# Kernel tuning notes

Hardware: AMD Instinct MI355X
Metric: run time of the kernel (lower is better)

Reference implementation:

```python
import jax, jax.numpy as jnp
import numpy as np
import math

B, S, P, G = 8, 512, 64, 64
E, GE = 768, 32          # sub_embed_dim, gene_embed_dim
HD = E // 2              # sub_head_dim = 384
L = P * G
LAMBDA_INIT = 0.8 - 0.6 * math.exp(-0.3 * 0)  # depth=0 -> 0.2
SCALING = HD ** -0.5


def setup_inputs() -> dict:
    key0 = jax.random.key(0)
    ks = jax.random.split(key0, 12)
    init = 0.02
    return {
        "query": jax.random.normal(ks[0], (B, S, E), jnp.float32),
        "key": jax.random.normal(ks[1], (B, P, G, GE), jnp.float32),
        "query_mask": jax.random.bernoulli(ks[2], 0.9, (B, S)),
        "key_mask": jax.random.bernoulli(ks[3], 0.9, (B, P, G)),
        # weights stored [in, out] so y = x @ W (equiv to torch Linear no-bias)
        "Wq": jax.random.normal(ks[4], (E, E), jnp.float32) * init,
        "Wkv": jax.random.normal(ks[5], (GE, 2 * E), jnp.float32) * init,
        "Wout": jax.random.normal(ks[6], (E, E), jnp.float32) * init,
        "lambda_q1": jax.random.normal(ks[7], (HD,), jnp.float32) * 0.1,
        "lambda_k1": jax.random.normal(ks[8], (HD,), jnp.float32) * 0.1,
        "lambda_q2": jax.random.normal(ks[9], (HD,), jnp.float32) * 0.1,
        "lambda_k2": jax.random.normal(ks[10], (HD,), jnp.float32) * 0.1,
        "ln_weight": jnp.ones((E,), jnp.float32),  # RMSNorm affine weight (2*HD = E)
    }


def reference(query, key, query_mask, key_mask, Wq, Wkv, Wout,
              lambda_q1, lambda_k1, lambda_q2, lambda_k2, ln_weight):
    # Projections
    Q = query @ Wq                                   # [B,S,E]
    KV = key.reshape(B, L, GE) @ Wkv                 # [B,L,2E]
    K = KV[..., :E]                                  # [B,L,E]
    V = KV[..., E:]                                  # [B,L,E] (= 2*HD)

    # Split into 2 heads of dim HD
    Qh = Q.reshape(B, S, 2, HD).transpose(0, 2, 1, 3) * SCALING   # [B,2,S,HD]
    Kh = K.reshape(B, L, 2, HD).transpose(0, 2, 1, 3)             # [B,2,L,HD]

    # Combined mask [B,S,L]
    mask = query_mask[:, :, None] & key_mask.reshape(B, L)[:, None, :]

    # Dual attention scores + stable softmax (eps=1e-8 on denominator)
    scores = jnp.einsum('bhsd,bhld->bhsl', Qh, Kh)                # [B,2,S,L]
    scores = jnp.where(mask[:, None], scores, -1e20)
    m = jnp.max(scores, axis=-1, keepdims=True)
    p = jnp.exp(scores - m)
    attn = p / (jnp.sum(p, axis=-1, keepdims=True) + 1e-8)

    # Differential combination
    lam = (jnp.exp(jnp.sum(lambda_q1 * lambda_k1))
           - jnp.exp(jnp.sum(lambda_q2 * lambda_k2)) + LAMBDA_INIT)
    diff = attn[:, 0] - lam * attn[:, 1]                          # [B,S,L]
    diff = diff - jnp.min(diff, axis=-1, keepdims=True) + 1e-20
    diff = jnp.where(mask, diff, 0.0)

    # Value contraction: [B,S,L] @ [B,L,E] -> [B,S,E]
    attn_out = jnp.einsum('bsl,ble->bse', diff, V)

    # RMSNorm (eps=1e-5, affine) then scale by (1 - lambda_init)
    ms = jnp.mean(attn_out * attn_out, axis=-1, keepdims=True)
    attn_out = attn_out * jax.lax.rsqrt(ms + 1e-5) * ln_weight
    attn_out = attn_out * (1.0 - LAMBDA_INIT)

    out = attn_out @ Wout                                         # [B,S,E]
    return out, diff.reshape(B, S, P, G)
```

## Files before the change

### kernel.cpp

```cpp
#include <hip/hip_runtime.h>
#include <math.h>

#define LAM_INIT 0.2f
#define ONE_MINUS_LAM 0.8f
#define SCALING_F 0.05103103630798288f

typedef _Float16 h2 __attribute__((ext_vector_type(2)));

#if defined(__has_builtin)
#if __has_builtin(__builtin_amdgcn_fdot2)
#define FDOT2(a, b, c) __builtin_amdgcn_fdot2((a), (b), (c), false)
#endif
#endif
#ifndef FDOT2
#define FDOT2(a, b, c) ((float)(a).x * (float)(b).x + ((float)(a).y * (float)(b).y + (c)))
#endif

__device__ inline float waveMax(float v) {
#pragma unroll
    for (int o = 32; o > 0; o >>= 1) v = fmaxf(v, __shfl_xor(v, o));
    return v;
}
__device__ inline float waveMin(float v) {
#pragma unroll
    for (int o = 32; o > 0; o >>= 1) v = fminf(v, __shfl_xor(v, o));
    return v;
}
__device__ inline float waveSum(float v) {
#pragma unroll
    for (int o = 32; o > 0; o >>= 1) v += __shfl_xor(v, o);
    return v;
}

__global__ __launch_bounds__(256) void k01_prep(
    const float* __restrict__ key, const float* __restrict__ Wq,
    const float* __restrict__ Wkv, const float* __restrict__ Wout,
    const float* __restrict__ lq1, const float* __restrict__ lk1,
    const float* __restrict__ lq2, const float* __restrict__ lk2,
    const float* __restrict__ ln,
    unsigned* __restrict__ keyThU, float* __restrict__ Wcp,
    float* __restrict__ Wvp, float* __restrict__ lam)
{
    int blk = blockIdx.x;
    int tid = threadIdx.x;
    if (blk < 128) {
        int b  = blk >> 4;
        int l0 = (blk & 15) << 8;
        __shared__ float tile[256 * 33];
        const float* kp = key + ((size_t)b * 4096 + l0) * 32;
#pragma unroll
        for (int q = 0; q < 32; ++q) {
            int idx = tid + (q << 8);
            int r = idx >> 5, g = idx & 31;
            tile[r * 33 + g] = kp[idx];
        }
        __syncthreads();
#pragma unroll
        for (int gp = 0; gp < 16; ++gp) {
            h2 v;
            v.x = (_Float16)tile[tid * 33 + 2 * gp];
            v.y = (_Float16)tile[tid * 33 + 2 * gp + 1];
            keyThU[((size_t)(b * 16 + gp)) * 4096 + l0 + tid] =
                __builtin_bit_cast(unsigned, v);
        }
    } else if (blk < 512) {
        int bb = blk - 128;
        int kc = bb & 1;
        int ob = bb >> 1;
        int idx = ob * 256 + tid;
        int e  = idx >> 6;
        int hg = idx & 63;
        int h = hg >> 5, g = hg & 31;
        const float4* wqr = (const float4*)(Wq  + (size_t)e * 768 + h * 384 + kc * 192);
        const float4* wkr = (const float4*)(Wkv + (size_t)g * 1536 + h * 384 + kc * 192);
        float s0 = 0.f, s1 = 0.f;
#pragma unroll 4
        for (int d = 0; d < 48; d += 2) {
            float4 a0 = wqr[d],   b0 = wkr[d];
            float4 a1 = wqr[d+1], b1 = wkr[d+1];
            s0 += a0.x*b0.x + a0.y*b0.y + a0.z*b0.z + a0.w*b0.w;
            s1 += a1.x*b1.x + a1.y*b1.y + a1.z*b1.z + a1.w*b1.w;
        }
        Wcp[kc * 49152 + idx] = (s0 + s1) * SCALING_F;
    } else if (blk < 1280) {
        int bb = blk - 512;
        int kc = bb / 96;
        int ob = bb - kc * 96;
        int idx = ob * 256 + tid;
        int g = idx / 768;
        int e = idx - g * 768;
        const float* wvr = Wkv + (size_t)g * 1536 + 768;
        int c0 = kc * 96;
        float s0 = 0.f, s1 = 0.f;
#pragma unroll 4
        for (int c = c0; c < c0 + 96; c += 2) {
            s0 += wvr[c]   * ln[c]   * Wout[(size_t)c * 768 + e];
            s1 += wvr[c+1] * ln[c+1] * Wout[(size_t)(c+1) * 768 + e];
        }
        Wvp[kc * 24576 + idx] = s0 + s1;
    } else {
        float s1 = 0.f, s2 = 0.f;
        for (int d = tid; d < 384; d += 256) {
            s1 += lq1[d] * lk1[d];
            s2 += lq2[d] * lk2[d];
        }
        s1 = waveSum(s1);
        s2 = waveSum(s2);
        __shared__ float r1[4], r2[4];
        int wid = tid >> 6, lane = tid & 63;
        if (lane == 0) { r1[wid] = s1; r2[wid] = s2; }
        __syncthreads();
        if (tid == 0) {
            float a  = r1[0] + r1[1] + r1[2] + r1[3];
            float b2 = r2[0] + r2[1] + r2[2] + r2[3];
            lam[0] = expf(a) - expf(b2) + LAM_INIT;
        }
    }
}

__global__ __launch_bounds__(256) void k2_qt(
    const float* __restrict__ query, const float* __restrict__ Wcp,
    const float* __restrict__ Wvp, float* __restrict__ Wvo,
    float* __restrict__ Qtp)
{
    int blk = blockIdx.x;
    int tid = threadIdx.x;
    if (blk >= 512) {
        int idx = (blk - 512) * 256 + tid;
        float s = 0.f;
#pragma unroll
        for (int kc = 0; kc < 8; ++kc) s += Wvp[kc * 24576 + idx];
        Wvo[idx] = s;
        return;
    }
    int kc = blk >> 7;
    int mt = blk & 127;
    int m0 = mt * 32;
    __shared__ __align__(16) float As[64 * 33];
    __shared__ __align__(16) float Bs[64 * 64];

    int tm = tid >> 5;
    int tn = tid & 31;
    float acc[4][2];
#pragma unroll
    for (int r = 0; r < 4; ++r) { acc[r][0] = 0.f; acc[r][1] = 0.f; }

    for (int ch = 0; ch < 3; ++ch) {
        int k0 = kc * 192 + ch * 64;
        __syncthreads();
#pragma unroll
        for (int q = 0; q < 2; ++q) {
            int f = tid + q * 256;
            int m = f >> 4, kq = f & 15;
            float4 v = *(const float4*)&query[(size_t)(m0 + m) * 768 + k0 + kq * 4];
            As[(kq * 4 + 0) * 33 + m] = v.x;
            As[(kq * 4 + 1) * 33 + m] = v.y;
            As[(kq * 4 + 2) * 33 + m] = v.z;
            As[(kq * 4 + 3) * 33 + m] = v.w;
        }
#pragma unroll
        for (int q = 0; q < 4; ++q) {
            int f = tid + q * 256;
            int kk = f >> 4, n4 = f & 15;
            float4 a = *(const float4*)&Wcp[(size_t)(k0 + kk) * 64 + n4 * 4];
            float4 b = *(const float4*)&Wcp[49152 + (size_t)(k0 + kk) * 64 + n4 * 4];
            float4 s; s.x = a.x + b.x; s.y = a.y + b.y; s.z = a.z + b.z; s.w = a.w + b.w;
            *(float4*)&Bs[kk * 64 + n4 * 4] = s;
        }
        __syncthreads();
#pragma unroll 8
        for (int kk = 0; kk < 64; ++kk) {
            float4 a = *(const float4*)&As[kk * 33 + tm * 4];
            float2 b = *(const float2*)&Bs[kk * 64 + tn * 2];
            acc[0][0] += a.x * b.x; acc[0][1] += a.x * b.y;
            acc[1][0] += a.y * b.x; acc[1][1] += a.y * b.y;
            acc[2][0] += a.z * b.x; acc[2][1] += a.z * b.y;
            acc[3][0] += a.w * b.x; acc[3][1] += a.w * b.y;
        }
    }
#pragma unroll
    for (int r = 0; r < 4; ++r) {
        float2 o; o.x = acc[r][0]; o.y = acc[r][1];
        *(float2*)&Qtp[(size_t)kc * 262144 + (size_t)(m0 + tm * 4 + r) * 64 + tn * 2] = o;
    }
}

__global__ __launch_bounds__(512, 4) void k3_attn(
    const float* __restrict__ Qtp, const unsigned* __restrict__ keyThU,
    const int* __restrict__ qmask, const int* __restrict__ kmask,
    const float* __restrict__ lamp, float* __restrict__ diffO)
{
    int blk = blockIdx.x;
    int b  = blk >> 7;
    int s0 = (blk & 127) * 4;
    int tid = threadIdx.x;
    int lane = tid & 63, wid = tid >> 6;

    __shared__ __align__(16) unsigned qt_th[128];
    __shared__ float red[64];

    if (tid < 128) {
        int ts = tid >> 5;
        int h  = (tid >> 4) & 1;
        int gp = tid & 15;
        size_t row = (size_t)(b * 512 + s0 + ts) * 64;
        int col = h * 32 + 2 * gp;
        float v0 = 0.f, v1 = 0.f;
#pragma unroll
        for (int kc = 0; kc < 4; ++kc) {
            v0 += Qtp[(size_t)kc * 262144 + row + col];
            v1 += Qtp[(size_t)kc * 262144 + row + col + 1];
        }
        h2 hv; hv.x = (_Float16)v0; hv.y = (_Float16)v1;
        qt_th[gp * 8 + ts * 2 + h] = __builtin_bit_cast(unsigned, hv);
    }
    int qm[4];
#pragma unroll
    for (int ts = 0; ts < 4; ++ts) qm[ts] = qmask[b * 512 + s0 + ts];
    float lam = lamp[0];

    unsigned kmb = 0;
#pragma unroll
    for (int c = 0; c < 2; ++c) {
        int4 km = *(const int4*)(kmask + b * 4096 + c * 2048 + tid * 4);
        if (km.x) kmb |= 1u << (c * 4 + 0);
        if (km.y) kmb |= 1u << (c * 4 + 1);
        if (km.z) kmb |= 1u << (c * 4 + 2);
        if (km.w) kmb |= 1u << (c * 4 + 3);
    }
    __syncthreads();

    float p[2][4][8];
#pragma unroll
    for (int h = 0; h < 2; ++h)
#pragma unroll
        for (int ts = 0; ts < 4; ++ts)
#pragma unroll
            for (int i = 0; i < 8; ++i) p[h][ts][i] = 0.f;

    const unsigned* kt = keyThU + (size_t)b * 16 * 4096 + tid * 4;
    for (int gp = 0; gp < 16; ++gp) {
        uint4 q0 = *(const uint4*)&qt_th[gp * 8];
        uint4 q1 = *(const uint4*)&qt_th[gp * 8 + 4];
        h2 qv[8];
        qv[0] = __builtin_bit_cast(h2, q0.x); qv[1] = __builtin_bit_cast(h2, q0.y);
        qv[2] = __builtin_bit_cast(h2, q0.z); qv[3] = __builtin_bit_cast(h2, q0.w);
        qv[4] = __builtin_bit_cast(h2, q1.x); qv[5] = __builtin_bit_cast(h2, q1.y);
        qv[6] = __builtin_bit_cast(h2, q1.z); qv[7] = __builtin_bit_cast(h2, q1.w);
        const unsigned* kg = kt + (size_t)gp * 4096;
#pragma unroll
        for (int c = 0; c < 2; ++c) {
            uint4 kv = *(const uint4*)(kg + c * 2048);
            h2 k0 = __builtin_bit_cast(h2, kv.x);
            h2 k1 = __builtin_bit_cast(h2, kv.y);
            h2 k2 = __builtin_bit_cast(h2, kv.z);
            h2 k3 = __builtin_bit_cast(h2, kv.w);
#pragma unroll
            for (int ts = 0; ts < 4; ++ts)
#pragma unroll
                for (int h = 0; h < 2; ++h) {
                    h2 q = qv[ts * 2 + h];
                    p[h][ts][c*4+0] = FDOT2(k0, q, p[h][ts][c*4+0]);
                    p[h][ts][c*4+1] = FDOT2(k1, q, p[h][ts][c*4+1]);
                    p[h][ts][c*4+2] = FDOT2(k2, q, p[h][ts][c*4+2]);
                    p[h][ts][c*4+3] = FDOT2(k3, q, p[h][ts][c*4+3]);
                }
        }
    }

#pragma unroll
    for (int h = 0; h < 2; ++h)
#pragma unroll
        for (int ts = 0; ts < 4; ++ts)
#pragma unroll
            for (int i = 0; i < 8; ++i) {
                bool ok = qm[ts] && ((kmb >> i) & 1u);
                p[h][ts][i] = ok ? p[h][ts][i] : -1e20f;
            }

    float mrow[2][4];
#pragma unroll
    for (int h = 0; h < 2; ++h)
#pragma unroll
        for (int ts = 0; ts < 4; ++ts) {
            float v = -3.4e38f;
#pragma unroll
            for (int i = 0; i < 8; ++i) v = fmaxf(v, p[h][ts][i]);
            v = waveMax(v);
            if (lane == 0) red[(h * 4 + ts) * 8 + wid] = v;
        }
    __syncthreads();
#pragma unroll
    for (int h = 0; h < 2; ++h)
#pragma unroll
        for (int ts = 0; ts < 4; ++ts) {
            int r = (h * 4 + ts) * 8;
            float v = red[r];
#pragma unroll
            for (int w = 1; w < 8; ++w) v = fmaxf(v, red[r + w]);
            mrow[h][ts] = v;
        }
    __syncthreads();

    float inv[2][4];
#pragma unroll
    for (int h = 0; h < 2; ++h)
#pragma unroll
        for (int ts = 0; ts < 4; ++ts) {
            float s = 0.f;
#pragma unroll
            for (int i = 0; i < 8; ++i) {
                float e2 = __expf(p[h][ts][i] - mrow[h][ts]);
                p[h][ts][i] = e2;
                s += e2;
            }
            s = waveSum(s);
            if (lane == 0) red[(h * 4 + ts) * 8 + wid] = s;
        }
    __syncthreads();
#pragma unroll
    for (int h = 0; h < 2; ++h)
#pragma unroll
        for (int ts = 0; ts < 4; ++ts) {
            int r = (h * 4 + ts) * 8;
            float s = red[r];
#pragma unroll
            for (int w = 1; w < 8; ++w) s += red[r + w];
            inv[h][ts] = 1.0f / (s + 1e-8f);
        }
    __syncthreads();

    float mn[4];
#pragma unroll
    for (int ts = 0; ts < 4; ++ts) {
        float v = 3.4e38f;
#pragma unroll
        for (int i = 0; i < 8; ++i) {
            float d = p[0][ts][i] * inv[0][ts] - lam * (p[1][ts][i] * inv[1][ts]);
            p[0][ts][i] = d;
            v = fminf(v, d);
        }
        v = waveMin(v);
        if (lane == 0) red[ts * 8 + wid] = v;
    }
    __syncthreads();
#pragma unroll
    for (int ts = 0; ts < 4; ++ts) {
        int r = ts * 8;
        float v = red[r];
#pragma unroll
        for (int w = 1; w < 8; ++w) v = fminf(v, red[r + w]);
        mn[ts] = v;
    }

#pragma unroll
    for (int ts = 0; ts < 4; ++ts) {
        size_t base = (size_t)(b * 512 + s0 + ts) * 4096 + tid * 4;
#pragma unroll
        for (int c = 0; c < 2; ++c) {
            float4 o;
            float v0 = p[0][ts][c*4+0] - mn[ts] + 1e-20f;
            float v1 = p[0][ts][c*4+1] - mn[ts] + 1e-20f;
            float v2 = p[0][ts][c*4+2] - mn[ts] + 1e-20f;
            float v3 = p[0][ts][c*4+3] - mn[ts] + 1e-20f;
            o.x = (qm[ts] && ((kmb >> (c*4+0)) & 1u)) ? v0 : 0.f;
            o.y = (qm[ts] && ((kmb >> (c*4+1)) & 1u)) ? v1 : 0.f;
            o.z = (qm[ts] && ((kmb >> (c*4+2)) & 1u)) ? v2 : 0.f;
            o.w = (qm[ts] && ((kmb >> (c*4+3)) & 1u)) ? v3 : 0.f;
            *(float4*)(diffO + base + c * 2048) = o;
        }
    }
}

__global__ __launch_bounds__(256) void k4_T(
    const float* __restrict__ diff, const float* __restrict__ key,
    float* __restrict__ P)
{
    int blk = blockIdx.x;
    int rt = blk & 63, kc = blk >> 6;
    int row0 = rt << 6;
    int b = row0 >> 9;
    int l0 = kc << 9;
    int tid = threadIdx.x;
    int tx = tid & 7;
    int ty = tid >> 3;
    int g0 = tx * 4;

    __shared__ __align__(16) float Ks[256][32];

    float acc[2][4];
#pragma unroll
    for (int r = 0; r < 2; ++r)
#pragma unroll
        for (int c2 = 0; c2 < 4; ++c2) acc[r][c2] = 0.f;

    for (int ph = 0; ph < 2; ++ph) {
        int lp = l0 + ph * 256;
        __syncthreads();
#pragma unroll
        for (int q = 0; q < 32; ++q) {
            int idx = tid + (q << 8);
            int r = idx >> 5, g = idx & 31;
            Ks[r][g] = key[((size_t)(b * 4096 + lp + r)) * 32 + g];
        }
        __syncthreads();

        for (int j4 = 0; j4 < 64; ++j4) {
            int l = lp + j4 * 4;
            float4 dv[2];
#pragma unroll
            for (int r = 0; r < 2; ++r)
                dv[r] = *(const float4*)(diff + (size_t)(row0 + ty * 2 + r) * 4096 + l);
#pragma unroll
            for (int jj = 0; jj < 4; ++jj) {
                float4 kq = *(const float4*)&Ks[j4 * 4 + jj][g0];
#pragma unroll
                for (int r = 0; r < 2; ++r) {
                    float d = (jj == 0) ? dv[r].x : (jj == 1) ? dv[r].y : (jj == 2) ? dv[r].z : dv[r].w;
                    acc[r][0] += d * kq.x;
                    acc[r][1] += d * kq.y;
                    acc[r][2] += d * kq.z;
                    acc[r][3] += d * kq.w;
                }
            }
        }
    }
#pragma unroll
    for (int r = 0; r < 2; ++r) {
        float4 o; o.x = acc[r][0]; o.y = acc[r][1]; o.z = acc[r][2]; o.w = acc[r][3];
        *(float4*)&P[(size_t)kc * 131072 + (size_t)(row0 + ty * 2 + r) * 32 + g0] = o;
    }
}

__global__ __launch_bounds__(256) void k5_out(
    const float* __restrict__ P, const float* __restrict__ Wkv,
    const float* __restrict__ Wvo, float* __restrict__ out)
{
    int row0 = blockIdx.x * 8;
    int tid = threadIdx.x;
    int wid = tid >> 6, lane = tid & 63;
    __shared__ __align__(16) float Ts[8][32];
    __shared__ float red[8][4];
    __shared__ float rs_s[8];

    {
        int r = tid >> 5, g = tid & 31;
        float s = 0.f;
#pragma unroll
        for (int kc = 0; kc < 8; ++kc)
            s += P[(size_t)kc * 131072 + (size_t)(row0 + r) * 32 + g];
        Ts[r][g] = s;
    }
    __syncthreads();

    float ssq[8];
#pragma unroll
    for (int r = 0; r < 8; ++r) ssq[r] = 0.f;

#pragma unroll
    for (int ec = 0; ec < 3; ++ec) {
        int e = tid + ec * 256;
        float wv[32];
#pragma unroll
        for (int g = 0; g < 32; ++g) wv[g] = Wkv[(size_t)g * 1536 + 768 + e];
#pragma unroll
        for (int r = 0; r < 8; ++r) {
            float a = 0.f;
#pragma unroll
            for (int g = 0; g < 32; ++g) a += Ts[r][g] * wv[g];
            ssq[r] += a * a;
        }
    }
#pragma unroll
    for (int r = 0; r < 8; ++r) {
        float v = waveSum(ssq[r]);
        if (lane == 0) red[r][wid] = v;
    }
    __syncthreads();
    if (tid < 8) {
        float s = red[tid][0] + red[tid][1] + red[tid][2] + red[tid][3];
        float ms = s * (1.0f / 768.0f);
        rs_s[tid] = rsqrtf(ms + 1e-5f) * ONE_MINUS_LAM;
    }
    __syncthreads();

#pragma unroll
    for (int ec = 0; ec < 3; ++ec) {
        int e = tid + ec * 256;
        float wo[32];
#pragma unroll
        for (int g = 0; g < 32; ++g) wo[g] = Wvo[(size_t)g * 768 + e];
#pragma unroll
        for (int r = 0; r < 8; ++r) {
            float o = 0.f;
#pragma unroll
            for (int g = 0; g < 32; ++g) o += Ts[r][g] * wo[g];
            out[(size_t)(row0 + r) * 768 + e] = o * rs_s[r];
        }
    }
}

extern "C" void kernel_launch(void* const* d_in, const int* in_sizes, int n_in,
                              void* d_out, int out_size, void* d_ws, size_t ws_size,
                              hipStream_t stream) {
    (void)in_sizes; (void)n_in; (void)out_size; (void)ws_size;
    const float* query = (const float*)d_in[0];
    const float* key   = (const float*)d_in[1];
    const int*   qmask = (const int*)d_in[2];
    const int*   kmask = (const int*)d_in[3];
    const float* Wq    = (const float*)d_in[4];
    const float* Wkv   = (const float*)d_in[5];
    const float* Wout  = (const float*)d_in[6];
    const float* lq1   = (const float*)d_in[7];
    const float* lk1   = (const float*)d_in[8];
    const float* lq2   = (const float*)d_in[9];
    const float* lk2   = (const float*)d_in[10];
    const float* ln    = (const float*)d_in[11];

    float* out  = (float*)d_out;
    float* diff = out + 3145728;

    float* ws      = (float*)d_ws;
    float* Wcp     = ws;
    float* Wvo     = ws + 98304;
    float* Wvp     = ws + 122880;
    float* lam     = ws + 319488;
    unsigned* keyThU = (unsigned*)(ws + 319552);
    float* Qtp     = ws + 843840;
    float* P       = Qtp;

    k01_prep<<<1281, 256, 0, stream>>>(key, Wq, Wkv, Wout, lq1, lk1, lq2, lk2, ln,
                                       keyThU, Wcp, Wvp, lam);
    k2_qt<<<608, 256, 0, stream>>>(query, Wcp, Wvp, Wvo, Qtp);
    k3_attn<<<1024, 512, 0, stream>>>(Qtp, keyThU, qmask, kmask, lam, diff);
    k4_T<<<512, 256, 0, stream>>>(diff, key, P);
    k5_out<<<512, 256, 0, stream>>>(P, Wkv, Wvo, out);
}
```

Measured before the change: 234.7 us.

## Drop softmax max reduction, halve query rows per attention block, prefetch keys

The attention kernel now handles 2 query rows per block instead of 4 and launches twice as many blocks. It removes the row-max reduction and its block barriers by exponentiating raw scores directly, zeroing masked entries instead of using a -1e20 fill. It also register-prefetches the next key group and uses nontemporal loads and stores for the Q partials and the diff output. Skipping the max subtraction assumes scores stay small enough not to overflow exp. Fewer rows per block means each block re-reads the full key tile, which doubles key traffic.

Measured after the change: 439.0 us. 1.87x slower.

```diff
diff --git a/kernel.cpp b/kernel.cpp
--- a/kernel.cpp
+++ b/kernel.cpp
@@ -6,6 +6,7 @@
 #define SCALING_F 0.05103103630798288f
 
 typedef _Float16 h2 __attribute__((ext_vector_type(2)));
+typedef float f4 __attribute__((ext_vector_type(4)));
 
 #if defined(__has_builtin)
 #if __has_builtin(__builtin_amdgcn_fdot2)
@@ -16,11 +17,6 @@
 #define FDOT2(a, b, c) ((float)(a).x * (float)(b).x + ((float)(a).y * (float)(b).y + (c)))
 #endif
 
-__device__ inline float waveMax(float v) {
-#pragma unroll
-    for (int o = 32; o > 0; o >>= 1) v = fmaxf(v, __shfl_xor(v, o));
-    return v;
-}
 __device__ inline float waveMin(float v) {
 #pragma unroll
     for (int o = 32; o > 0; o >>= 1) v = fminf(v, __shfl_xor(v, o));
@@ -191,15 +187,16 @@
     const float* __restrict__ lamp, float* __restrict__ diffO)
 {
     int blk = blockIdx.x;
-    int b  = blk >> 7;
-    int s0 = (blk & 127) * 4;
+    int b  = blk >> 8;
+    int s0 = (blk & 255) * 2;
     int tid = threadIdx.x;
     int lane = tid & 63, wid = tid >> 6;
 
-    __shared__ __align__(16) unsigned qt_th[128];
-    __shared__ float red[64];
-
-    if (tid < 128) {
+    __shared__ __align__(16) unsigned qt_th[64];
+    __shared__ float redS[32];
+    __shared__ float redM[16];
+
+    if (tid < 64) {
         int ts = tid >> 5;
         int h  = (tid >> 4) & 1;
         int gp = tid & 15;
@@ -208,15 +205,15 @@
         float v0 = 0.f, v1 = 0.f;
 #pragma unroll
         for (int kc = 0; kc < 4; ++kc) {
-            v0 += Qtp[(size_t)kc * 262144 + row + col];
-            v1 += Qtp[(size_t)kc * 262144 + row + col + 1];
+            v0 += __builtin_nontemporal_load(Qtp + (size_t)kc * 262144 + row + col);
+            v1 += __builtin_nontemporal_load(Qtp + (size_t)kc * 262144 + row + col + 1);
         }
         h2 hv; hv.x = (_Float16)v0; hv.y = (_Float16)v1;
-        qt_th[gp * 8 + ts * 2 + h] = __builtin_bit_cast(unsigned, hv);
-    }
-    int qm[4];
-#pragma unroll
-    for (int ts = 0; ts < 4; ++ts) qm[ts] = qmask[b * 512 + s0 + ts];
+        qt_th[gp * 4 + ts * 2 + h] = __builtin_bit_cast(unsigned, hv);
+    }
+    int qm[2];
+    qm[0] = qmask[b * 512 + s0];
+    qm[1] = qmask[b * 512 + s0 + 1];
     float lam = lamp[0];
 
     unsigned kmb = 0;
@@ -230,109 +227,85 @@
     }
     __syncthreads();
 
-    float p[2][4][8];
+    float p[2][2][8];
 #pragma unroll
     for (int h = 0; h < 2; ++h)
 #pragma unroll
-        for (int ts = 0; ts < 4; ++ts)
+        for (int ts = 0; ts < 2; ++ts)
 #pragma unroll
             for (int i = 0; i < 8; ++i) p[h][ts][i] = 0.f;
 
-    const unsigned* kt = keyThU + (size_t)b * 16 * 4096 + tid * 4;
+    const unsigned* kt = keyThU + (size_t)b * 65536 + tid * 4;
+    uint4 ka = *(const uint4*)(kt);
+    uint4 kb = *(const uint4*)(kt + 2048);
     for (int gp = 0; gp < 16; ++gp) {
-        uint4 q0 = *(const uint4*)&qt_th[gp * 8];
-        uint4 q1 = *(const uint4*)&qt_th[gp * 8 + 4];
-        h2 qv[8];
-        qv[0] = __builtin_bit_cast(h2, q0.x); qv[1] = __builtin_bit_cast(h2, q0.y);
-        qv[2] = __builtin_bit_cast(h2, q0.z); qv[3] = __builtin_bit_cast(h2, q0.w);
-        qv[4] = __builtin_bit_cast(h2, q1.x); qv[5] = __builtin_bit_cast(h2, q1.y);
-        qv[6] = __builtin_bit_cast(h2, q1.z); qv[7] = __builtin_bit_cast(h2, q1.w);
-        const unsigned* kg = kt + (size_t)gp * 4096;
-#pragma unroll
-        for (int c = 0; c < 2; ++c) {
-            uint4 kv = *(const uint4*)(kg + c * 2048);
-            h2 k0 = __builtin_bit_cast(h2, kv.x);
-            h2 k1 = __builtin_bit_cast(h2, kv.y);
-            h2 k2 = __builtin_bit_cast(h2, kv.z);
-            h2 k3 = __builtin_bit_cast(h2, kv.w);
-#pragma unroll
-            for (int ts = 0; ts < 4; ++ts)
-#pragma unroll
-                for (int h = 0; h < 2; ++h) {
-                    h2 q = qv[ts * 2 + h];
-                    p[h][ts][c*4+0] = FDOT2(k0, q, p[h][ts][c*4+0]);
-                    p[h][ts][c*4+1] = FDOT2(k1, q, p[h][ts][c*4+1]);
-                    p[h][ts][c*4+2] = FDOT2(k2, q, p[h][ts][c*4+2]);
-                    p[h][ts][c*4+3] = FDOT2(k3, q, p[h][ts][c*4+3]);
-                }
-        }
-    }
-
+        uint4 q0 = *(const uint4*)&qt_th[gp * 4];
+        uint4 kva = ka, kvb = kb;
+        if (gp < 15) {
+            const unsigned* kn = kt + (gp + 1) * 4096;
+            ka = *(const uint4*)(kn);
+            kb = *(const uint4*)(kn + 2048);
+        }
+        h2 qv[4];
+        qv[0] = __builtin_bit_cast(h2, q0.x);
+        qv[1] = __builtin_bit_cast(h2, q0.y);
+        qv[2] = __builtin_bit_cast(h2, q0.z);
+        qv[3] = __builtin_bit_cast(h2, q0.w);
+        h2 a0 = __builtin_bit_cast(h2, kva.x);
+        h2 a1 = __builtin_bit_cast(h2, kva.y);
+        h2 a2 = __builtin_bit_cast(h2, kva.z);
+        h2 a3 = __builtin_bit_cast(h2, kva.w);
+        h2 c0 = __builtin_bit_cast(h2, kvb.x);
+        h2 c1 = __builtin_bit_cast(h2, kvb.y);
+        h2 c2 = __builtin_bit_cast(h2, kvb.z);
+        h2 c3 = __builtin_bit_cast(h2, kvb.w);
+#pragma unroll
+        for (int ts = 0; ts < 2; ++ts)
+#pragma unroll
+            for (int h = 0; h < 2; ++h) {
+                h2 q = qv[ts * 2 + h];
+                p[h][ts][0] = FDOT2(a0, q, p[h][ts][0]);
+                p[h][ts][1] = FDOT2(a1, q, p[h][ts][1]);
+                p[h][ts][2] = FDOT2(a2, q, p[h][ts][2]);
+                p[h][ts][3] = FDOT2(a3, q, p[h][ts][3]);
+                p[h][ts][4] = FDOT2(c0, q, p[h][ts][4]);
+                p[h][ts][5] = FDOT2(c1, q, p[h][ts][5]);
+                p[h][ts][6] = FDOT2(c2, q, p[h][ts][6]);
+                p[h][ts][7] = FDOT2(c3, q, p[h][ts][7]);
+            }
+    }
+
+    float inv[2][2];
 #pragma unroll
     for (int h = 0; h < 2; ++h)
 #pragma unroll
-        for (int ts = 0; ts < 4; ++ts)
+        for (int ts = 0; ts < 2; ++ts) {
+            float s = 0.f;
 #pragma unroll
             for (int i = 0; i < 8; ++i) {
                 bool ok = qm[ts] && ((kmb >> i) & 1u);
-                p[h][ts][i] = ok ? p[h][ts][i] : -1e20f;
-            }
-
-    float mrow[2][4];
-#pragma unroll
-    for (int h = 0; h < 2; ++h)
-#pragma unroll
-        for (int ts = 0; ts < 4; ++ts) {
-            float v = -3.4e38f;
-#pragma unroll
-            for (int i = 0; i < 8; ++i) v = fmaxf(v, p[h][ts][i]);
-            v = waveMax(v);
-            if (lane == 0) red[(h * 4 + ts) * 8 + wid] = v;
-        }
-    __syncthreads();
-#pragma unroll
-    for (int h = 0; h < 2; ++h)
-#pragma unroll
-        for (int ts = 0; ts < 4; ++ts) {
-            int r = (h * 4 + ts) * 8;
-            float v = red[r];
-#pragma unroll
-            for (int w = 1; w < 8; ++w) v = fmaxf(v, red[r + w]);
-            mrow[h][ts] = v;
-        }
-    __syncthreads();
-
-    float inv[2][4];
-#pragma unroll
-    for (int h = 0; h < 2; ++h)
-#pragma unroll
-        for (int ts = 0; ts < 4; ++ts) {
-            float s = 0.f;
-#pragma unroll
-            for (int i = 0; i < 8; ++i) {
-                float e2 = __expf(p[h][ts][i] - mrow[h][ts]);
-                p[h][ts][i] = e2;
-                s += e2;
+                float e = ok ? __expf(p[h][ts][i]) : 0.f;
+                p[h][ts][i] = e;
+                s += e;
             }
             s = waveSum(s);
-            if (lane == 0) red[(h * 4 + ts) * 8 + wid] = s;
+            if (lane == 0) redS[(h * 2 + ts) * 8 + wid] = s;
         }
     __syncthreads();
 #pragma unroll
     for (int h = 0; h < 2; ++h)
 #pragma unroll
-        for (int ts = 0; ts < 4; ++ts) {
-            int r = (h * 4 + ts) * 8;
-            float s = red[r];
-#pragma unroll
-            for (int w = 1; w < 8; ++w) s += red[r + w];
+        for (int ts = 0; ts < 2; ++ts) {
+            int r = (h * 2 + ts) * 8;
+            float s = redS[r];
+#pragma unroll
+            for (int w = 1; w < 8; ++w) s += redS[r + w];
             inv[h][ts] = 1.0f / (s + 1e-8f);
         }
-    __syncthreads();
-
-    float mn[4];
-#pragma unroll
-    for (int ts = 0; ts < 4; ++ts) {
+
+    float mn[2];
+#pragma unroll
+    for (int ts = 0; ts < 2; ++ts) {
         float v = 3.4e38f;
 #pragma unroll
         for (int i = 0; i < 8; ++i) {
@@ -341,33 +314,33 @@
             v = fminf(v, d);
         }
         v = waveMin(v);
-        if (lane == 0) red[ts * 8 + wid] = v;
+        if (lane == 0) redM[ts * 8 + wid] = v;
     }
     __syncthreads();
 #pragma unroll
-    for (int ts = 0; ts < 4; ++ts) {
-        int r = ts * 8;
-        float v = red[r];
-#pragma unroll
-        for (int w = 1; w < 8; ++w) v = fminf(v, red[r + w]);
+    for (int ts = 0; ts < 2; ++ts) {
+        float v = redM[ts * 8];
+#pragma unroll
+        for (int w = 1; w < 8; ++w) v = fminf(v, redM[ts * 8 + w]);
         mn[ts] = v;
     }
 
 #pragma unroll
-    for (int ts = 0; ts < 4; ++ts) {
+    for (int ts = 0; ts < 2; ++ts) {
         size_t base = (size_t)(b * 512 + s0 + ts) * 4096 + tid * 4;
+        bool q_ = qm[ts] != 0;
 #pragma unroll
         for (int c = 0; c < 2; ++c) {
-            float4 o;
+            f4 o;
             float v0 = p[0][ts][c*4+0] - mn[ts] + 1e-20f;
             float v1 = p[0][ts][c*4+1] - mn[ts] + 1e-20f;
             float v2 = p[0][ts][c*4+2] - mn[ts] + 1e-20f;
             float v3 = p[0][ts][c*4+3] - mn[ts] + 1e-20f;
-            o.x = (qm[ts] && ((kmb >> (c*4+0)) & 1u)) ? v0 : 0.f;
-            o.y = (qm[ts] && ((kmb >> (c*4+1)) & 1u)) ? v1 : 0.f;
-            o.z = (qm[ts] && ((kmb >> (c*4+2)) & 1u)) ? v2 : 0.f;
-            o.w = (qm[ts] && ((kmb >> (c*4+3)) & 1u)) ? v3 : 0.f;
-            *(float4*)(diffO + base + c * 2048) = o;
+            o.x = (q_ && ((kmb >> (c*4+0)) & 1u)) ? v0 : 0.f;
+            o.y = (q_ && ((kmb >> (c*4+1)) & 1u)) ? v1 : 0.f;
+            o.z = (q_ && ((kmb >> (c*4+2)) & 1u)) ? v2 : 0.f;
+            o.w = (q_ && ((kmb >> (c*4+3)) & 1u)) ? v3 : 0.f;
+            __builtin_nontemporal_store(o, (f4*)(diffO + base + c * 2048));
         }
     }
 }
@@ -407,10 +380,11 @@
 
         for (int j4 = 0; j4 < 64; ++j4) {
             int l = lp + j4 * 4;
-            float4 dv[2];
+            f4 dv[2];
 #pragma unroll
             for (int r = 0; r < 2; ++r)
-                dv[r] = *(const float4*)(diff + (size_t)(row0 + ty * 2 + r) * 4096 + l);
+                dv[r] = __builtin_nontemporal_load(
+                    (const f4*)(diff + (size_t)(row0 + ty * 2 + r) * 4096 + l));
 #pragma unroll
             for (int jj = 0; jj < 4; ++jj) {
                 float4 kq = *(const float4*)&Ks[j4 * 4 + jj][g0];
@@ -532,7 +506,7 @@
     k01_prep<<<1281, 256, 0, stream>>>(key, Wq, Wkv, Wout, lq1, lk1, lq2, lk2, ln,
                                        keyThU, Wcp, Wvp, lam);
     k2_qt<<<608, 256, 0, stream>>>(query, Wcp, Wvp, Wvo, Qtp);
-    k3_attn<<<1024, 512, 0, stream>>>(Qtp, keyThU, qmask, kmask, lam, diff);
+    k3_attn<<<2048, 512, 0, stream>>>(Qtp, keyThU, qmask, kmask, lam, diff);
     k4_T<<<512, 256, 0, stream>>>(diff, key, P);
     k5_out<<<512, 256, 0, stream>>>(P, Wkv, Wvo, out);
 }
```
